# Kernel tuning notes

Measured on AMD Instinct MI355X. Metric: run time of the kernel, lower is better.

The kernel has to match this reference:

```python
import jax, jax.numpy as jnp
import numpy as np

D_MODEL = 768
N_HEADS = 12
HEAD_DIM = D_MODEL // N_HEADS
BATCH = 1
SEQ = 4096


def setup_inputs() -> dict:
    key = jax.random.key(0)
    ks = jax.random.split(key, 5)
    std = 1.0 / np.sqrt(D_MODEL)
    return {
        "x": jax.random.normal(ks[0], (BATCH, SEQ, D_MODEL), dtype=jnp.float32),
        "Wq": jax.random.normal(ks[1], (D_MODEL, D_MODEL), dtype=jnp.float32) * std,
        "Wk": jax.random.normal(ks[2], (D_MODEL, D_MODEL), dtype=jnp.float32) * std,
        "Wv": jax.random.normal(ks[3], (D_MODEL, D_MODEL), dtype=jnp.float32) * std,
        "Wp": jax.random.normal(ks[4], (D_MODEL, D_MODEL), dtype=jnp.float32) * std,
    }


def reference(x, Wq, Wk, Wv, Wp):
    B, S, D = x.shape
    scale = HEAD_DIM ** -0.5
    # torch Linear: y = x @ W.T ; reshape to [B, H, S, hd]
    def split_heads(y):
        return y.reshape(B, S, N_HEADS, HEAD_DIM).transpose(0, 2, 1, 3)
    q = split_heads(x @ Wq.T)
    k = split_heads(x @ Wk.T)
    v = split_heads(x @ Wv.T)
    # full [B, H, S, S] scores, as in the original module
    att = jnp.einsum("bhqd,bhkd->bhqk", q, k) * scale
    causal = jnp.tril(jnp.ones((S, S), dtype=bool))
    att = jnp.where(causal[None, None], att, -jnp.inf)
    att = jax.nn.softmax(att, axis=-1)
    y = jnp.einsum("bhqk,bhkd->bhqd", att, v)
    y = y.transpose(0, 2, 1, 3).reshape(B, S, D)
    return y @ Wp.T
```

## Files before the change

### kernel.cpp

```cpp
#include <hip/hip_runtime.h>
#include <hip/hip_bf16.h>
#include <stdint.h>

#define DM 768
#define SQ 4096
#define NH 12

typedef __bf16 bf16;
typedef __bf16 bf16x8 __attribute__((ext_vector_type(8)));
typedef float floatx4 __attribute__((ext_vector_type(4)));
typedef short short4v __attribute__((ext_vector_type(4)));

#if defined(__has_builtin)
#if __has_builtin(__builtin_amdgcn_mfma_f32_16x16x16bf16_1k)
#define HAVE_MFMA16 1
#endif
#endif
#ifndef HAVE_MFMA16
#define HAVE_MFMA16 0
#endif

typedef __attribute__((address_space(1))) const uint32_t cu32_g;
typedef __attribute__((address_space(3))) uint32_t u32_l;

__device__ __forceinline__ uint16_t f2bf(float f) {
  uint32_t u = __builtin_bit_cast(uint32_t, f);
  u += 0x7fff + ((u >> 16) & 1);
  return (uint16_t)(u >> 16);
}

__device__ __forceinline__ uint32_t pk2(float lo, float hi) {
  __hip_bfloat162 h = __float22bfloat162_rn(float2{lo, hi});
  uint32_t u;
  __builtin_memcpy(&u, &h, 4);
  return u;
}

__device__ __forceinline__ float bflo(uint32_t u) {
  return __builtin_bit_cast(float, u << 16);
}
__device__ __forceinline__ float bfhi(uint32_t u) {
  return __builtin_bit_cast(float, u & 0xffff0000u);
}

__device__ __forceinline__ void async16(const bf16* g, bf16* l) {
  __builtin_amdgcn_global_load_lds((cu32_g*)g, (u32_l*)l, 16, 0, 0);
}

__global__ __launch_bounds__(256) void cvt_kernel(
    const float* __restrict__ x, const float* __restrict__ wq,
    const float* __restrict__ wk, const float* __restrict__ wv,
    const float* __restrict__ wp, bf16* __restrict__ xb, bf16* __restrict__ wqb,
    bf16* __restrict__ wkb, bf16* __restrict__ wvb, bf16* __restrict__ wpb) {
  const int XQ = (SQ * DM) / 4;
  const int WQ = (DM * DM) / 4;
  int t = blockIdx.x * 256 + threadIdx.x;
  const float* src;
  bf16* dst;
  int local;
  if (t < XQ) { src = x;  dst = xb;  local = t; }
  else if (t < XQ + WQ)     { src = wq; dst = wqb; local = t - XQ; }
  else if (t < XQ + 2 * WQ) { src = wk; dst = wkb; local = t - XQ - WQ; }
  else if (t < XQ + 3 * WQ) { src = wv; dst = wvb; local = t - XQ - 2 * WQ; }
  else                      { src = wp; dst = wpb; local = t - XQ - 3 * WQ; }
  float4 v = ((const float4*)src)[local];
  ushort4 o;
  o.x = f2bf(v.x); o.y = f2bf(v.y); o.z = f2bf(v.z); o.w = f2bf(v.w);
  ((ushort4*)dst)[local] = o;
}

__device__ __forceinline__ void gemm_core(const bf16* __restrict__ A,
                                          const bf16* __restrict__ B, int m0,
                                          int n0, floatx4 (&acc)[4][4]) {
  __shared__ bf16 lA[2 * 4096];
  __shared__ bf16 lB[2 * 4096];
  const int tid = threadIdx.x;
  const int lane = tid & 63;
  const int w = tid >> 6;

  const int r0 = w * 32 + (lane >> 2);
  const int ke = (((lane & 3) ^ ((lane >> 3) & 3))) * 8;
  const bf16* gA0 = A + (size_t)(m0 + r0) * DM + ke;
  const bf16* gA1 = A + (size_t)(m0 + r0 + 16) * DM + ke;
  const bf16* gB0 = B + (size_t)(n0 + r0) * DM + ke;
  const bf16* gB1 = B + (size_t)(n0 + r0 + 16) * DM + ke;

  async16(gA0, lA + w * 1024); async16(gA1, lA + w * 1024 + 512);
  async16(gB0, lB + w * 1024); async16(gB1, lB + w * 1024 + 512);
  gA0 += 32; gA1 += 32; gB0 += 32; gB1 += 32;

  const int mrow = (w >> 1) * 64 + (lane & 15);
  const int nrow = (w & 1) * 64 + (lane & 15);
  const int cswz = ((lane >> 4) ^ ((lane >> 1) & 3)) * 8;

  for (int kt = 0; kt < DM / 32; ++kt) {
    __syncthreads();
    if (kt + 1 < DM / 32) {
      const int nb = ((kt + 1) & 1) * 4096;
      async16(gA0, lA + nb + w * 1024); async16(gA1, lA + nb + w * 1024 + 512);
      async16(gB0, lB + nb + w * 1024); async16(gB1, lB + nb + w * 1024 + 512);
      gA0 += 32; gA1 += 32; gB0 += 32; gB1 += 32;
    }
    const int cb = (kt & 1) * 4096;
    bf16x8 a[4], b[4];
#pragma unroll
    for (int mt = 0; mt < 4; ++mt)
      a[mt] = *(const bf16x8*)&lA[cb + (mrow + mt * 16) * 32 + cswz];
#pragma unroll
    for (int nt = 0; nt < 4; ++nt)
      b[nt] = *(const bf16x8*)&lB[cb + (nrow + nt * 16) * 32 + cswz];
#pragma unroll
    for (int mt = 0; mt < 4; ++mt)
#pragma unroll
      for (int nt = 0; nt < 4; ++nt)
        acc[mt][nt] = __builtin_amdgcn_mfma_f32_16x16x32_bf16(
            a[mt], b[nt], acc[mt][nt], 0, 0, 0);
  }
}

__global__ __launch_bounds__(256) void qkv_kernel(
    const bf16* __restrict__ xb, const bf16* __restrict__ wq,
    const bf16* __restrict__ wk, const bf16* __restrict__ wv,
    bf16* __restrict__ Qb, bf16* __restrict__ Kb, bf16* __restrict__ Vtb) {
  const int z = blockIdx.z;
  const bf16* B = (z == 0) ? wq : (z == 1) ? wk : wv;
  const int m0 = blockIdx.x * 128, n0 = blockIdx.y * 128;
  floatx4 acc[4][4] = {};
  gemm_core(xb, B, m0, n0, acc);
  const int lane = threadIdx.x & 63, w = threadIdx.x >> 6;
  const int quad = lane >> 4, ql = lane & 15;
  const float qs = (z == 0) ? 0.18033688011112042f : 1.0f;
  if (z < 2) {
    bf16* C = (z == 0) ? Qb : Kb;
#pragma unroll
    for (int mt = 0; mt < 4; ++mt)
#pragma unroll
      for (int nt = 0; nt < 4; ++nt) {
        int row = m0 + (w >> 1) * 64 + mt * 16 + quad * 4;
        int col = n0 + (w & 1) * 64 + nt * 16 + ql;
#pragma unroll
        for (int r = 0; r < 4; ++r)
          *(uint16_t*)&C[(size_t)(row + r) * DM + col] = f2bf(acc[mt][nt][r] * qs);
      }
  } else {
#pragma unroll
    for (int mt = 0; mt < 4; ++mt)
#pragma unroll
      for (int nt = 0; nt < 4; ++nt) {
        int row = m0 + (w >> 1) * 64 + mt * 16 + quad * 4;
        int col = n0 + (w & 1) * 64 + nt * 16 + ql;
        uint32_t lo = pk2(acc[mt][nt][0], acc[mt][nt][1]);
        uint32_t hi = pk2(acc[mt][nt][2], acc[mt][nt][3]);
        *(uint2*)&Vtb[(size_t)col * SQ + row] = make_uint2(lo, hi);
      }
  }
}

__global__ __launch_bounds__(256) void proj_kernel(
    const bf16* __restrict__ Ob, const bf16* __restrict__ wp,
    float* __restrict__ out) {
  __shared__ bf16 lA[2 * 2048];
  __shared__ bf16 lB[2 * 4096];
  const int tid = threadIdx.x, lane = tid & 63, w = tid >> 6;
  const int m0 = blockIdx.x * 64, n0 = blockIdx.y * 128;

  const int ke = (((lane & 3) ^ ((lane >> 3) & 3))) * 8;
  const bf16* gA = Ob + (size_t)(m0 + w * 16 + (lane >> 2)) * DM + ke;
  const bf16* gB0 = wp + (size_t)(n0 + w * 32 + (lane >> 2)) * DM + ke;
  const bf16* gB1 = wp + (size_t)(n0 + w * 32 + (lane >> 2) + 16) * DM + ke;

  async16(gA, lA + w * 512);
  async16(gB0, lB + w * 1024); async16(gB1, lB + w * 1024 + 512);
  gA += 32; gB0 += 32; gB1 += 32;

  const int mrow = (w >> 1) * 32 + (lane & 15);
  const int nrow = (w & 1) * 64 + (lane & 15);
  const int cswz = ((lane >> 4) ^ ((lane >> 1) & 3)) * 8;
  floatx4 acc[2][4] = {};

  for (int kt = 0; kt < DM / 32; ++kt) {
    __syncthreads();
    if (kt + 1 < DM / 32) {
      const int nbA = ((kt + 1) & 1) * 2048, nbB = ((kt + 1) & 1) * 4096;
      async16(gA, lA + nbA + w * 512);
      async16(gB0, lB + nbB + w * 1024); async16(gB1, lB + nbB + w * 1024 + 512);
      gA += 32; gB0 += 32; gB1 += 32;
    }
    const int cbA = (kt & 1) * 2048, cbB = (kt & 1) * 4096;
    bf16x8 a[2], b[4];
#pragma unroll
    for (int mt = 0; mt < 2; ++mt)
      a[mt] = *(const bf16x8*)&lA[cbA + (mrow + mt * 16) * 32 + cswz];
#pragma unroll
    for (int nt = 0; nt < 4; ++nt)
      b[nt] = *(const bf16x8*)&lB[cbB + (nrow + nt * 16) * 32 + cswz];
#pragma unroll
    for (int mt = 0; mt < 2; ++mt)
#pragma unroll
      for (int nt = 0; nt < 4; ++nt)
        acc[mt][nt] = __builtin_amdgcn_mfma_f32_16x16x32_bf16(
            a[mt], b[nt], acc[mt][nt], 0, 0, 0);
  }
  const int quad = lane >> 4, ql = lane & 15;
#pragma unroll
  for (int mt = 0; mt < 2; ++mt)
#pragma unroll
    for (int nt = 0; nt < 4; ++nt) {
      int row = m0 + (w >> 1) * 32 + mt * 16 + quad * 4;
      int col = n0 + (w & 1) * 64 + nt * 16 + ql;
#pragma unroll
      for (int r = 0; r < 4; ++r)
        out[(size_t)(row + r) * DM + col] = acc[mt][nt][r];
    }
}

__global__ __launch_bounds__(256) void attn_kernel(
    const bf16* __restrict__ Qb, const bf16* __restrict__ Kb,
    const bf16* __restrict__ Vtb, uint16_t* __restrict__ OpartB,
    float* __restrict__ Lpart, bf16* __restrict__ Ob) {
#if HAVE_MFMA16
  __shared__ __align__(16) char smem[65536];
#else
  __shared__ __align__(16) char smem[73728];
  bf16* lPt = (bf16*)(smem + 65536);
#endif
  const int tid = threadIdx.x, lane = tid & 63, w = tid >> 6;
  const int quad = lane >> 4, ql = lane & 15;

  int b = blockIdx.x;
  int h = b % NH;
  int i = b / NH;
  int qb, c;
  if (i < 32)      { qb = 31 - (i >> 2); c = i & 3; }
  else if (i < 56) { int t2 = i - 32; qb = 23 - t2 / 3; c = t2 % 3; }
  else if (i < 72) { int t2 = i - 56; qb = 15 - (t2 >> 1); c = t2 & 1; }
  else             { qb = 79 - i; c = 0; }
  const int kv0 = c * 1024;
  const int kv_end = min((qb + 1) * 128, kv0 + 1024);
  const int n_it = (kv_end - kv0) >> 7;
  const bool diag = (kv_end == (qb + 1) * 128);

  bf16x8 qf[2][2];
#pragma unroll
  for (int nt = 0; nt < 2; ++nt)
#pragma unroll
    for (int kt = 0; kt < 2; ++kt)
      qf[nt][kt] = *(const bf16x8*)&Qb[(size_t)(qb * 128 + w * 32 + nt * 16 + ql) * DM +
                                       h * 64 + kt * 32 + quad * 8];

  const int src_e = (((lane & 3) ^ ((lane >> 3) & 3))) * 8;
  const bf16* gK[4];
  const bf16* gV4[4];
#pragma unroll
  for (int t = 0; t < 4; ++t) {
    int o = t * 4096 + w * 1024 + lane * 16;
    int cK = o >> 13, rK = (o & 8191) >> 6;
    gK[t] = Kb + (size_t)(kv0 + rK) * DM + h * 64 + cK * 32 + src_e;
    int dV = w * 16 + (lane >> 2);
    gV4[t] = Vtb + (size_t)(h * 64 + dV) * SQ + kv0 + t * 32 + src_e;
  }

#pragma unroll
  for (int t = 0; t < 4; ++t) {
    async16(gK[t], (bf16*)(smem + t * 4096 + w * 1024));
    async16(gV4[t], (bf16*)(smem + 16384 + t * 4096 + w * 1024));
    gK[t] += 128 * DM;
    gV4[t] += 128;
  }

  floatx4 o_acc[4][2] = {};
  float l_s[2] = {0.f, 0.f};
  const int cswz = ((lane >> 4) ^ ((lane >> 1) & 3)) * 8;

  for (int j = 0; j < n_it; ++j) {
    __syncthreads();
    if (j + 1 < n_it) {
      char* dst = smem + ((j + 1) & 1) * 32768;
#pragma unroll
      for (int t = 0; t < 4; ++t) {
        async16(gK[t], (bf16*)(dst + t * 4096 + w * 1024));
        async16(gV4[t], (bf16*)(dst + 16384 + t * 4096 + w * 1024));
        gK[t] += 128 * DM;
        gV4[t] += 128;
      }
    }
    const char* cbuf = smem + (j & 1) * 32768;
    const bf16* kbuf = (const bf16*)cbuf;
    const char* vbuf = cbuf + 16384;

    floatx4 s[8][2] = {};
#pragma unroll
    for (int kt = 0; kt < 2; ++kt)
#pragma unroll
      for (int mt = 0; mt < 8; ++mt) {
        bf16x8 a = *(const bf16x8*)&kbuf[kt * 4096 + (mt * 16 + ql) * 32 + cswz];
#pragma unroll
        for (int nt = 0; nt < 2; ++nt)
          s[mt][nt] = __builtin_amdgcn_mfma_f32_16x16x32_bf16(a, qf[nt][kt],
                                                              s[mt][nt], 0, 0, 0);
      }

    if (diag && j == n_it - 1) {
#pragma unroll
      for (int mt = 0; mt < 8; ++mt)
#pragma unroll
        for (int nt = 0; nt < 2; ++nt)
#pragma unroll
          for (int r = 0; r < 4; ++r) {
            int kpos = mt * 16 + quad * 4 + r;
            int qpos = w * 32 + nt * 16 + ql;
            if (kpos > qpos) s[mt][nt][r] = -1e30f;
          }
    }

    uint2 pp[8][2];
#pragma unroll
    for (int nt = 0; nt < 2; ++nt) {
      float tsum[8];
#pragma unroll
      for (int mt = 0; mt < 8; ++mt) {
        float p0 = __builtin_amdgcn_exp2f(s[mt][nt][0]);
        float p1 = __builtin_amdgcn_exp2f(s[mt][nt][1]);
        float p2 = __builtin_amdgcn_exp2f(s[mt][nt][2]);
        float p3 = __builtin_amdgcn_exp2f(s[mt][nt][3]);
        pp[mt][nt] = make_uint2(pk2(p0, p1), pk2(p2, p3));
        tsum[mt] = (p0 + p1) + (p2 + p3);
      }
      l_s[nt] += ((tsum[0] + tsum[1]) + (tsum[2] + tsum[3])) +
                 ((tsum[4] + tsum[5]) + (tsum[6] + tsum[7]));
    }

#if HAVE_MFMA16
#pragma unroll
    for (int mt = 0; mt < 8; ++mt) {
      short4v bfr[2];
#pragma unroll
      for (int nt = 0; nt < 2; ++nt) {
        union { uint2 u; short4v v; } pb;
        pb.u = pp[mt][nt];
        bfr[nt] = pb.v;
      }
      const char* vbase = vbuf + (mt >> 1) * 4096 +
          ((((mt & 1) * 2 + (quad >> 1)) ^ ((ql >> 1) & 3)) * 16) +
          (quad & 1) * 8;
#pragma unroll
      for (int mtd = 0; mtd < 4; ++mtd) {
        short4v a = *(const short4v*)(vbase + (mtd * 16 + ql) * 64);
#pragma unroll
        for (int nt = 0; nt < 2; ++nt)
          o_acc[mtd][nt] = __builtin_amdgcn_mfma_f32_16x16x16bf16_1k(
              a, bfr[nt], o_acc[mtd][nt], 0, 0, 0);
      }
    }
#else
    bf16* lp = lPt + w * 1024;
#pragma unroll
    for (int ks = 0; ks < 4; ++ks) {
#pragma unroll
      for (int nt = 0; nt < 2; ++nt) {
        int q32 = nt * 16 + ql;
        int key = (q32 >> 1) & 7;
#pragma unroll
        for (int mtp = 0; mtp < 2; ++mtp) {
          int slot = mtp * 4 + quad;
          *(uint2*)((char*)lp + q32 * 64 + ((slot ^ key) * 8)) = pp[2 * ks + mtp][nt];
        }
      }
      bf16x8 bp[2];
#pragma unroll
      for (int nt = 0; nt < 2; ++nt) {
        int q32 = nt * 16 + ql;
        int key = (q32 >> 1) & 7;
        union { uint2 u[2]; bf16x8 v; } pb;
        pb.u[0] = *(uint2*)((char*)lp + q32 * 64 + (((2 * quad) ^ key) * 8));
        pb.u[1] = *(uint2*)((char*)lp + q32 * 64 + (((2 * quad + 1) ^ key) * 8));
        bp[nt] = pb.v;
      }
#pragma unroll
      for (int mtd = 0; mtd < 4; ++mtd) {
        bf16x8 a = *(const bf16x8*)((const bf16*)vbuf + ks * 2048 +
                                    (mtd * 16 + ql) * 32 + cswz);
#pragma unroll
        for (int nt = 0; nt < 2; ++nt)
          o_acc[mtd][nt] = __builtin_amdgcn_mfma_f32_16x16x32_bf16(
              a, bp[nt], o_acc[mtd][nt], 0, 0, 0);
      }
    }
#endif
  }

  float lf[2];
#pragma unroll
  for (int nt = 0; nt < 2; ++nt) {
    float ls = l_s[nt];
    ls += __shfl_xor(ls, 16);
    ls += __shfl_xor(ls, 32);
    lf[nt] = ls;
  }

  if (kv0 == 0 && diag) {
#pragma unroll
    for (int nt = 0; nt < 2; ++nt) {
      float rl = 1.0f / lf[nt];
      int qg = qb * 128 + w * 32 + nt * 16 + ql;
#pragma unroll
      for (int mtd = 0; mtd < 4; ++mtd) {
        uint32_t lo = pk2(o_acc[mtd][nt][0] * rl, o_acc[mtd][nt][1] * rl);
        uint32_t hi = pk2(o_acc[mtd][nt][2] * rl, o_acc[mtd][nt][3] * rl);
        *(uint2*)&Ob[(size_t)qg * DM + h * 64 + mtd * 16 + quad * 4] =
            make_uint2(lo, hi);
      }
    }
  } else {
    const int ps = (h * 32 + qb) * 4 + c;
#pragma unroll
    for (int nt = 0; nt < 2; ++nt) {
      int q = w * 32 + nt * 16 + ql;
      if (quad == 0) Lpart[ps * 128 + q] = lf[nt];
#pragma unroll
      for (int mtd = 0; mtd < 4; ++mtd) {
        uint32_t lo = pk2(o_acc[mtd][nt][0], o_acc[mtd][nt][1]);
        uint32_t hi = pk2(o_acc[mtd][nt][2], o_acc[mtd][nt][3]);
        *(uint2*)&OpartB[(size_t)ps * 8192 + q * 64 + mtd * 16 + quad * 4] =
            make_uint2(lo, hi);
      }
    }
  }
}

__global__ __launch_bounds__(256) void combine_kernel(
    const uint16_t* __restrict__ OpartB, const float* __restrict__ Lpart,
    bf16* __restrict__ Ob) {
  int b = blockIdx.x;
  int h = b % NH, qb = 8 + b / NH;
  int nch = (qb + 8) >> 3;
  int t = threadIdx.x;
  int q = t >> 1, dh = (t & 1) * 32;
  int ps0 = (h * 32 + qb) * 4;

  float acc[32] = {};
  float L = 0.f;
#pragma unroll
  for (int cc = 0; cc < 4; ++cc)
    if (cc < nch) {
      L += Lpart[(ps0 + cc) * 128 + q];
      const uint4* p =
          (const uint4*)(OpartB + (size_t)(ps0 + cc) * 8192 + q * 64 + dh);
#pragma unroll
      for (int g = 0; g < 4; ++g) {
        uint4 u = p[g];
        acc[g * 8 + 0] += bflo(u.x); acc[g * 8 + 1] += bfhi(u.x);
        acc[g * 8 + 2] += bflo(u.y); acc[g * 8 + 3] += bfhi(u.y);
        acc[g * 8 + 4] += bflo(u.z); acc[g * 8 + 5] += bfhi(u.z);
        acc[g * 8 + 6] += bflo(u.w); acc[g * 8 + 7] += bfhi(u.w);
      }
    }
  float rl = 1.0f / L;
  bf16* dst = &Ob[(size_t)(qb * 128 + q) * DM + h * 64 + dh];
#pragma unroll
  for (int g = 0; g < 4; ++g) {
    uint4 u;
    u.x = pk2(acc[g * 8 + 0] * rl, acc[g * 8 + 1] * rl);
    u.y = pk2(acc[g * 8 + 2] * rl, acc[g * 8 + 3] * rl);
    u.z = pk2(acc[g * 8 + 4] * rl, acc[g * 8 + 5] * rl);
    u.w = pk2(acc[g * 8 + 6] * rl, acc[g * 8 + 7] * rl);
    *(uint4*)&dst[g * 8] = u;
  }
}

extern "C" void kernel_launch(void* const* d_in, const int* in_sizes, int n_in,
                              void* d_out, int out_size, void* d_ws,
                              size_t ws_size, hipStream_t stream) {
  const float* x  = (const float*)d_in[0];
  const float* wq = (const float*)d_in[1];
  const float* wk = (const float*)d_in[2];
  const float* wv = (const float*)d_in[3];
  const float* wp = (const float*)d_in[4];
  char* ws = (char*)d_ws;
  float* Lpart = (float*)(ws);
  bf16* xb   = (bf16*)(ws);
  bf16* wqb  = (bf16*)(ws + 6291456);
  bf16* wkb  = (bf16*)(ws + 7471104);
  bf16* wvb  = (bf16*)(ws + 8650752);
  bf16* wpb  = (bf16*)(ws + 9830400);
  bf16* Qb   = (bf16*)(ws + 11010048);
  bf16* Kb   = (bf16*)(ws + 17301504);
  bf16* Vtb  = (bf16*)(ws + 23592960);
  bf16* Ob   = (bf16*)(ws + 29884416);
  uint16_t* OpartB = (uint16_t*)(ws + 36175872);

  cvt_kernel<<<5376, 256, 0, stream>>>(x, wq, wk, wv, wp, xb, wqb, wkb, wvb, wpb);
  qkv_kernel<<<dim3(32, 6, 3), 256, 0, stream>>>(xb, wqb, wkb, wvb, Qb, Kb, Vtb);
  attn_kernel<<<960, 256, 0, stream>>>(Qb, Kb, Vtb, OpartB, Lpart, Ob);
  combine_kernel<<<288, 256, 0, stream>>>(OpartB, Lpart, Ob);
  proj_kernel<<<dim3(64, 6), 256, 0, stream>>>(Ob, wpb, (float*)d_out);
}
```

Measured before the change: 175.9 us.

## Replace split-KV combine kernel with fp32 atomic accumulation and fold normalization into proj

Attention blocks now atomically add their unnormalized partial outputs and row sums into zeroed fp32 buffers instead of writing bf16 partials, which removes the combine kernel. The projection GEMM reads the fp32 output, divides by the accumulated row sum per head, converts to bf16 and stores it into LDS with register prefetch, replacing the async LDS load. This removes one launch and the partial-buffer round trip. In exchange it adds a memset, many scalar fp32 atomics (including for blocks that previously wrote directly), twice the bytes read by proj, and order-dependent summation.

```diff
diff --git a/kernel.cpp b/kernel.cpp
--- a/kernel.cpp
+++ b/kernel.cpp
@@ -34,13 +34,6 @@
   uint32_t u;
   __builtin_memcpy(&u, &h, 4);
   return u;
-}
-
-__device__ __forceinline__ float bflo(uint32_t u) {
-  return __builtin_bit_cast(float, u << 16);
-}
-__device__ __forceinline__ float bfhi(uint32_t u) {
-  return __builtin_bit_cast(float, u & 0xffff0000u);
 }
 
 __device__ __forceinline__ void async16(const bf16* g, bf16* l) {
@@ -157,21 +150,31 @@
 }
 
 __global__ __launch_bounds__(256) void proj_kernel(
-    const bf16* __restrict__ Ob, const bf16* __restrict__ wp,
-    float* __restrict__ out) {
+    const float* __restrict__ Of, const float* __restrict__ Lf,
+    const bf16* __restrict__ wp, float* __restrict__ out) {
   __shared__ bf16 lA[2 * 2048];
   __shared__ bf16 lB[2 * 4096];
   const int tid = threadIdx.x, lane = tid & 63, w = tid >> 6;
   const int m0 = blockIdx.x * 64, n0 = blockIdx.y * 128;
 
   const int ke = (((lane & 3) ^ ((lane >> 3) & 3))) * 8;
-  const bf16* gA = Ob + (size_t)(m0 + w * 16 + (lane >> 2)) * DM + ke;
+  const int r0v = w * 16 + (lane >> 2);
+  const float* gA = Of + (size_t)(m0 + r0v) * DM + ke;
+  const float* gL = Lf + (size_t)(m0 + r0v) * NH;
   const bf16* gB0 = wp + (size_t)(n0 + w * 32 + (lane >> 2)) * DM + ke;
   const bf16* gB1 = wp + (size_t)(n0 + w * 32 + (lane >> 2) + 16) * DM + ke;
 
-  async16(gA, lA + w * 512);
   async16(gB0, lB + w * 1024); async16(gB1, lB + w * 1024 + 512);
-  gA += 32; gB0 += 32; gB1 += 32;
+  gB0 += 32; gB1 += 32;
+  {
+    float4 a0 = *(const float4*)gA;
+    float4 a1 = *(const float4*)(gA + 4);
+    float rl = 1.0f / gL[ke >> 6];
+    uint4 u;
+    u.x = pk2(a0.x * rl, a0.y * rl); u.y = pk2(a0.z * rl, a0.w * rl);
+    u.z = pk2(a1.x * rl, a1.y * rl); u.w = pk2(a1.z * rl, a1.w * rl);
+    *(uint4*)&lA[tid * 8] = u;
+  }
 
   const int mrow = (w >> 1) * 32 + (lane & 15);
   const int nrow = (w & 1) * 64 + (lane & 15);
@@ -180,11 +183,17 @@
 
   for (int kt = 0; kt < DM / 32; ++kt) {
     __syncthreads();
-    if (kt + 1 < DM / 32) {
-      const int nbA = ((kt + 1) & 1) * 2048, nbB = ((kt + 1) & 1) * 4096;
-      async16(gA, lA + nbA + w * 512);
+    float4 a0, a1;
+    float rl;
+    const bool more = (kt + 1 < DM / 32);
+    if (more) {
+      const int nbB = ((kt + 1) & 1) * 4096;
       async16(gB0, lB + nbB + w * 1024); async16(gB1, lB + nbB + w * 1024 + 512);
-      gA += 32; gB0 += 32; gB1 += 32;
+      gB0 += 32; gB1 += 32;
+      int d0 = (kt + 1) * 32 + ke;
+      a0 = *(const float4*)(gA + (kt + 1) * 32);
+      a1 = *(const float4*)(gA + (kt + 1) * 32 + 4);
+      rl = 1.0f / gL[d0 >> 6];
     }
     const int cbA = (kt & 1) * 2048, cbB = (kt & 1) * 4096;
     bf16x8 a[2], b[4];
@@ -200,6 +209,13 @@
       for (int nt = 0; nt < 4; ++nt)
         acc[mt][nt] = __builtin_amdgcn_mfma_f32_16x16x32_bf16(
             a[mt], b[nt], acc[mt][nt], 0, 0, 0);
+    if (more) {
+      const int nbA = ((kt + 1) & 1) * 2048;
+      uint4 u;
+      u.x = pk2(a0.x * rl, a0.y * rl); u.y = pk2(a0.z * rl, a0.w * rl);
+      u.z = pk2(a1.x * rl, a1.y * rl); u.w = pk2(a1.z * rl, a1.w * rl);
+      *(uint4*)&lA[nbA + tid * 8] = u;
+    }
   }
   const int quad = lane >> 4, ql = lane & 15;
 #pragma unroll
@@ -216,8 +232,8 @@
 
 __global__ __launch_bounds__(256) void attn_kernel(
     const bf16* __restrict__ Qb, const bf16* __restrict__ Kb,
-    const bf16* __restrict__ Vtb, uint16_t* __restrict__ OpartB,
-    float* __restrict__ Lpart, bf16* __restrict__ Ob) {
+    const bf16* __restrict__ Vtb, float* __restrict__ Of,
+    float* __restrict__ Lf) {
 #if HAVE_MFMA16
   __shared__ __align__(16) char smem[65536];
 #else
@@ -398,73 +414,18 @@
     lf[nt] = ls;
   }
 
-  if (kv0 == 0 && diag) {
-#pragma unroll
-    for (int nt = 0; nt < 2; ++nt) {
-      float rl = 1.0f / lf[nt];
-      int qg = qb * 128 + w * 32 + nt * 16 + ql;
-#pragma unroll
-      for (int mtd = 0; mtd < 4; ++mtd) {
-        uint32_t lo = pk2(o_acc[mtd][nt][0] * rl, o_acc[mtd][nt][1] * rl);
-        uint32_t hi = pk2(o_acc[mtd][nt][2] * rl, o_acc[mtd][nt][3] * rl);
-        *(uint2*)&Ob[(size_t)qg * DM + h * 64 + mtd * 16 + quad * 4] =
-            make_uint2(lo, hi);
-      }
-    }
-  } else {
-    const int ps = (h * 32 + qb) * 4 + c;
-#pragma unroll
-    for (int nt = 0; nt < 2; ++nt) {
-      int q = w * 32 + nt * 16 + ql;
-      if (quad == 0) Lpart[ps * 128 + q] = lf[nt];
-#pragma unroll
-      for (int mtd = 0; mtd < 4; ++mtd) {
-        uint32_t lo = pk2(o_acc[mtd][nt][0], o_acc[mtd][nt][1]);
-        uint32_t hi = pk2(o_acc[mtd][nt][2], o_acc[mtd][nt][3]);
-        *(uint2*)&OpartB[(size_t)ps * 8192 + q * 64 + mtd * 16 + quad * 4] =
-            make_uint2(lo, hi);
-      }
-    }
-  }
-}
-
-__global__ __launch_bounds__(256) void combine_kernel(
-    const uint16_t* __restrict__ OpartB, const float* __restrict__ Lpart,
-    bf16* __restrict__ Ob) {
-  int b = blockIdx.x;
-  int h = b % NH, qb = 8 + b / NH;
-  int nch = (qb + 8) >> 3;
-  int t = threadIdx.x;
-  int q = t >> 1, dh = (t & 1) * 32;
-  int ps0 = (h * 32 + qb) * 4;
-
-  float acc[32] = {};
-  float L = 0.f;
-#pragma unroll
-  for (int cc = 0; cc < 4; ++cc)
-    if (cc < nch) {
-      L += Lpart[(ps0 + cc) * 128 + q];
-      const uint4* p =
-          (const uint4*)(OpartB + (size_t)(ps0 + cc) * 8192 + q * 64 + dh);
-#pragma unroll
-      for (int g = 0; g < 4; ++g) {
-        uint4 u = p[g];
-        acc[g * 8 + 0] += bflo(u.x); acc[g * 8 + 1] += bfhi(u.x);
-        acc[g * 8 + 2] += bflo(u.y); acc[g * 8 + 3] += bfhi(u.y);
-        acc[g * 8 + 4] += bflo(u.z); acc[g * 8 + 5] += bfhi(u.z);
-        acc[g * 8 + 6] += bflo(u.w); acc[g * 8 + 7] += bfhi(u.w);
-      }
-    }
-  float rl = 1.0f / L;
-  bf16* dst = &Ob[(size_t)(qb * 128 + q) * DM + h * 64 + dh];
-#pragma unroll
-  for (int g = 0; g < 4; ++g) {
-    uint4 u;
-    u.x = pk2(acc[g * 8 + 0] * rl, acc[g * 8 + 1] * rl);
-    u.y = pk2(acc[g * 8 + 2] * rl, acc[g * 8 + 3] * rl);
-    u.z = pk2(acc[g * 8 + 4] * rl, acc[g * 8 + 5] * rl);
-    u.w = pk2(acc[g * 8 + 6] * rl, acc[g * 8 + 7] * rl);
-    *(uint4*)&dst[g * 8] = u;
+#pragma unroll
+  for (int nt = 0; nt < 2; ++nt) {
+    int qg = qb * 128 + w * 32 + nt * 16 + ql;
+    if (quad == 0) atomicAdd(&Lf[qg * NH + h], lf[nt]);
+#pragma unroll
+    for (int mtd = 0; mtd < 4; ++mtd) {
+      float* dst = &Of[(size_t)qg * DM + h * 64 + mtd * 16 + quad * 4];
+      atomicAdd(dst + 0, o_acc[mtd][nt][0]);
+      atomicAdd(dst + 1, o_acc[mtd][nt][1]);
+      atomicAdd(dst + 2, o_acc[mtd][nt][2]);
+      atomicAdd(dst + 3, o_acc[mtd][nt][3]);
+    }
   }
 }
 
@@ -477,7 +438,6 @@
   const float* wv = (const float*)d_in[3];
   const float* wp = (const float*)d_in[4];
   char* ws = (char*)d_ws;
-  float* Lpart = (float*)(ws);
   bf16* xb   = (bf16*)(ws);
   bf16* wqb  = (bf16*)(ws + 6291456);
   bf16* wkb  = (bf16*)(ws + 7471104);
@@ -486,12 +446,12 @@
   bf16* Qb   = (bf16*)(ws + 11010048);
   bf16* Kb   = (bf16*)(ws + 17301504);
   bf16* Vtb  = (bf16*)(ws + 23592960);
-  bf16* Ob   = (bf16*)(ws + 29884416);
-  uint16_t* OpartB = (uint16_t*)(ws + 36175872);
-
+  float* Of  = (float*)(ws + 36175872);
+  float* Lf  = (float*)(ws + 48758784);
+
+  hipMemsetAsync(ws + 36175872, 0, 12582912 + 196608, stream);
   cvt_kernel<<<5376, 256, 0, stream>>>(x, wq, wk, wv, wp, xb, wqb, wkb, wvb, wpb);
   qkv_kernel<<<dim3(32, 6, 3), 256, 0, stream>>>(xb, wqb, wkb, wvb, Qb, Kb, Vtb);
-  attn_kernel<<<960, 256, 0, stream>>>(Qb, Kb, Vtb, OpartB, Lpart, Ob);
-  combine_kernel<<<288, 256, 0, stream>>>(OpartB, Lpart, Ob);
-  proj_kernel<<<dim3(64, 6), 256, 0, stream>>>(Ob, wpb, (float*)d_out);
-}
+  attn_kernel<<<960, 256, 0, stream>>>(Qb, Kb, Vtb, Of, Lf);
+  proj_kernel<<<dim3(64, 6), 256, 0, stream>>>(Of, Lf, wpb, (float*)d_out);
+}
```

Result: slower. 249.4 us (+41.8%).
